# Optimization experiments

Hardware: AMD Instinct MI355X
Metric: run time of the kernel (lower is better)

The kernel has to match this reference:

```python
import jax, jax.numpy as jnp
import numpy as np
from jax import lax

H = 64           # hid_size (hard-pinned by reshape(4,6,64) in source)
B = 16384        # number of months (prototype batch)
A = 16           # agent_num
N = B * A        # rows of `inputs`
P = 24           # num_prototypes = 4 * 6
T = 32           # jieqi_info sequence length
ACT = 12         # action_dim
EPS = 1e-4       # self.epsilon
BN_EPS = 1e-5
LN_EPS = 1e-5


def _lstm_step(h, c, x, w_ih, w_hh, b_ih, b_hh):
    # torch LSTM gate order: i, f, g, o
    g = x @ w_ih.T + h @ w_hh.T + b_ih + b_hh
    i, f, gg, o = jnp.split(g, 4, axis=-1)
    c = jax.nn.sigmoid(f) * c + jax.nn.sigmoid(i) * jnp.tanh(gg)
    h = jax.nn.sigmoid(o) * jnp.tanh(c)
    return h, c


def setup_inputs() -> dict:
    key = jax.random.key(0)
    ks = iter(jax.random.split(key, 40))

    def nrm(shape, s=0.05):
        return jax.random.normal(next(ks), shape, jnp.float32) * s

    inp = {
        "inputs": jax.random.normal(next(ks), (N, H), jnp.float32),
        "hidden_state": jax.random.normal(next(ks), (N, H), jnp.float32),
        "month": jax.random.randint(next(ks), (B,), 0, 12, jnp.int32),
        "jieqi_info": jax.random.normal(next(ks), (P, T, 3), jnp.float32),
        # bidirectional LSTM (input 3 -> hidden H), forward + backward dirs
        "w_ih_f": nrm((4 * H, 3)), "w_hh_f": nrm((4 * H, H)),
        "b_ih_f": nrm((4 * H,)), "b_hh_f": nrm((4 * H,)),
        "w_ih_b": nrm((4 * H, 3)), "w_hh_b": nrm((4 * H, H)),
        "b_ih_b": nrm((4 * H,)), "b_hh_b": nrm((4 * H,)),
        "fcl_w": nrm((H, 2 * H)), "fcl_b": nrm((H,)),      # jieqi_lstm_fc
        "proj_w": nrm((H, H)),                               # proto_proj (no bias)
        "conv_w": nrm((H, 2 * H)), "conv_b": nrm((H,)),    # conv_global
        "bn_g": jnp.ones((H,), jnp.float32), "bn_b": jnp.zeros((H,), jnp.float32),
        "fc1_w": nrm((H, H)), "fc1_b": nrm((H,)),
        "ln_g": jnp.ones((H,), jnp.float32), "ln_b": jnp.zeros((H,), jnp.float32),
        "gru_wih": nrm((3 * H, H)), "gru_whh": nrm((3 * H, H)),
        "gru_bih": nrm((3 * H,)), "gru_bhh": nrm((3 * H,)),
        "out_w": nrm((ACT, H)), "out_b": nrm((ACT,)),
    }
    # last_layer weight: +1 on correct class, -0.5 on incorrect (set_last_layer_incorrect_connection)
    ident = np.zeros((P, 4), np.float32)
    ident[np.arange(P), np.arange(P) // 6] = 1.0
    inp["last_w"] = jnp.asarray(1.0 * ident.T + (-0.5) * (1.0 - ident.T))  # [4, 24]
    return inp


def reference(inputs, hidden_state, month, jieqi_info,
              w_ih_f, w_hh_f, b_ih_f, b_hh_f,
              w_ih_b, w_hh_b, b_ih_b, b_hh_b,
              fcl_w, fcl_b, proj_w, last_w,
              conv_w, conv_b, bn_g, bn_b,
              fc1_w, fc1_b, ln_g, ln_b,
              gru_wih, gru_whh, gru_bih, gru_bhh,
              out_w, out_b):
    dt = inputs.dtype
    # ---- get_jieqi_prototype: biLSTM over [P, T, 3], take output at t=T-1 ----
    z0 = jnp.zeros((P, H), dt)

    def step(carry, x_t):
        h, c = carry
        h, c = _lstm_step(h, c, x_t, w_ih_f, w_hh_f, b_ih_f, b_hh_f)
        return (h, c), None

    (h_f, _), _ = lax.scan(step, (z0, z0), jnp.swapaxes(jieqi_info, 0, 1))
    # backward direction's output at the last time index = one step on x[:, -1]
    h_b, _ = _lstm_step(z0, z0, jieqi_info[:, -1, :], w_ih_b, w_hh_b, b_ih_b, b_hh_b)
    th = jnp.concatenate([h_f, h_b], axis=-1)                 # [P, 2H]
    pv = jax.nn.relu(th @ fcl_w.T + fcl_b) @ proj_w.T         # prototype_vectors [P, H]

    # ---- prototype_distances on full input batch ----
    xp = inputs @ pv.T                                        # [N, P]
    min_distances = (-2.0 * xp
                     + jnp.sum(inputs ** 2, axis=1, keepdims=True)
                     + jnp.sum(pv ** 2, axis=1)[None, :])
    prototype_activations = jnp.log((min_distances + 1.0) / (min_distances + EPS))
    logits = prototype_activations @ last_w.T                 # [N, 4]

    # ---- month -> season, select seasonal prototype block ----
    seasons = jnp.mod(jnp.floor_divide(month - 2, 3), 4)      # 2-4:0, 5-7:1, 8-10:2, else 3
    sub_proto = pv.reshape(4, 6, H)[seasons]                  # [B, 6, H]

    # ---- prototype_subgraph_distances (vectorized over the 6 protos) ----
    xr = inputs.reshape(B, A, H)
    d = jnp.sum((xr[:, None, :, :] - sub_proto[:, :, None, :]) ** 2, axis=-1)  # [B, 6, A]
    sim = jnp.mean(jnp.log((d + 1.0) / (d + EPS)), axis=2)    # [B, 6]

    # ---- argmax + gather + repeat ----
    chosen_idx = jnp.argmax(sim, axis=1)                      # [B]
    chosen = sub_proto[jnp.arange(B), chosen_idx]             # [B, H]
    chosen = jnp.broadcast_to(chosen[:, None, :], (B, A, H)).reshape(N, H)

    # ---- conv_global -> batchnorm(train) -> relu ----
    x_glb = jnp.concatenate([inputs, chosen], axis=-1) @ conv_w.T + conv_b
    mu = jnp.mean(x_glb, axis=0)
    var = jnp.mean((x_glb - mu) ** 2, axis=0)                 # biased, training-mode BN
    x_glb = (x_glb - mu) * lax.rsqrt(var + BN_EPS) * bn_g + bn_b
    x_glb = jax.nn.relu(x_glb)

    # ---- fc1 -> layernorm -> relu ----
    x = x_glb @ fc1_w.T + fc1_b
    lmu = jnp.mean(x, axis=-1, keepdims=True)
    lvar = jnp.mean((x - lmu) ** 2, axis=-1, keepdims=True)
    x = (x - lmu) * lax.rsqrt(lvar + LN_EPS) * ln_g + ln_b
    x = jax.nn.relu(x)

    # ---- GRUCell ----
    h_in = hidden_state.reshape(-1, H)
    gi = x @ gru_wih.T + gru_bih
    gh = h_in @ gru_whh.T + gru_bhh
    r = jax.nn.sigmoid(gi[:, :H] + gh[:, :H])
    zg = jax.nn.sigmoid(gi[:, H:2 * H] + gh[:, H:2 * H])
    n = jnp.tanh(gi[:, 2 * H:] + r * gh[:, 2 * H:])
    h = (1.0 - zg) * n + zg * h_in

    a = h @ out_w.T + out_b
    return (a, h, logits, min_distances)
```

## Files before the change

### kernel.cpp

```cpp
#include <hip/hip_runtime.h>
#include <cmath>

#define NHID 64
#define NMONTH 16384
#define NAGENT 16
#define NROWS (NMONTH*NAGENT)
#define NPROTO 24
#define TSEQ 32
#define NACT 12
#define EPS_P  1e-4f
#define EPS_BN 1e-5f
#define EPS_LN 1e-5f

typedef __attribute__((ext_vector_type(8))) short short8;
typedef __attribute__((ext_vector_type(4))) float f32x4;
typedef __attribute__((ext_vector_type(4))) unsigned short us4;
typedef __attribute__((ext_vector_type(8))) unsigned short us8;
typedef unsigned short ushort_t;

#define MFMA(a,b,c) __builtin_amdgcn_mfma_f32_16x16x32_bf16(a,b,c,0,0,0)
#define LPAD 68
#define LDSFENCE() asm volatile("s_waitcnt lgkmcnt(0)" ::: "memory")
#define LD8(P) (*reinterpret_cast<const short8*>(P))

typedef const __attribute__((address_space(1))) void* gvp;
typedef __attribute__((address_space(3))) void* lvp;

#define WS_PV     3072
#define WS_PVSQ   4608
#define WS_CTAB   4640
#define WS_MID1   6176
#define WS_MID2   14368
#define WS_BNSC   22560
#define WS_BNSH   22624
#define WS_WBF16  22688
#define WO_FC1   0
#define WO_GIH   4096
#define WO_GHH   16384
#define WO_OUT   28672
#define WO_PV    29696
#define WO_CVX   31744

__device__ __forceinline__ float sigf(float x){ return 1.0f/(1.0f+expf(-x)); }
__device__ __forceinline__ float fsig(float x){
  return __builtin_amdgcn_rcpf(1.f + __expf(-x));
}
__device__ __forceinline__ float ftanh(float x){
  return 1.f - 2.f*__builtin_amdgcn_rcpf(1.f + __expf(2.f*x));
}
__device__ __forceinline__ ushort_t f2bf(float f){
  unsigned u = __builtin_bit_cast(unsigned, f);
  u += 0x7FFFu + ((u>>16)&1u);
  return (ushort_t)(u>>16);
}
__device__ __forceinline__ float bf2f(ushort_t b){
  return __builtin_bit_cast(float, ((unsigned)b)<<16);
}
__device__ __forceinline__ unsigned pk2bf(float a, float b){
  unsigned d;
  asm("v_cvt_pk_bf16_f32 %0, %1, %2" : "=v"(d) : "v"(a), "v"(b));
  return d;
}
__device__ __forceinline__ ushort_t f2bf_hw(float x){
  unsigned d;
  asm("v_cvt_pk_bf16_f32 %0, %1, %2" : "=v"(d) : "v"(x), "v"(x));
  return (ushort_t)d;
}
__device__ __forceinline__ short8 hfrag(const float* hraw, int ra, int base){
  const int r15 = ra & 15;
  const float4 a = *reinterpret_cast<const float4*>(&hraw[ra*64 + (((base  )^r15)<<2)]);
  const float4 b = *reinterpret_cast<const float4*>(&hraw[ra*64 + (((base+1)^r15)<<2)]);
  uint4 u; u.x=pk2bf(a.x,a.y); u.y=pk2bf(a.z,a.w); u.z=pk2bf(b.x,b.y); u.w=pk2bf(b.z,b.w);
  return __builtin_bit_cast(short8, u);
}

__global__ __launch_bounds__(256) void k1_lstm(
    const float* __restrict__ jq,
    const float* __restrict__ wif, const float* __restrict__ whf,
    const float* __restrict__ bif, const float* __restrict__ bhf,
    const float* __restrict__ wib, const float* __restrict__ bib, const float* __restrict__ bhb,
    const float* __restrict__ fclw, const float* __restrict__ fclb,
    const float* __restrict__ projw, const float* __restrict__ convb,
    const float* __restrict__ fc1w, const float* __restrict__ gwih,
    const float* __restrict__ gwhh, const float* __restrict__ outw,
    const float* __restrict__ convw, ushort_t* __restrict__ wb,
    float* __restrict__ pvsq, float* __restrict__ ctab)
{
  __shared__ float hs[NHID];
  __shared__ float gs[4*NHID];
  if (blockIdx.x >= NPROTO){
    const int tt = (blockIdx.x - NPROTO)*256 + threadIdx.x;
    for (int i=tt;i<4096;i+=1024)  wb[WO_FC1+i]=f2bf(fc1w[i]);
    for (int i=tt;i<12288;i+=1024){ wb[WO_GIH+i]=f2bf(gwih[i]); wb[WO_GHH+i]=f2bf(gwhh[i]); }
    for (int i=tt;i<1024;i+=1024)  wb[WO_OUT+i] = (i<768)? f2bf(outw[i]) : (ushort_t)0;
    for (int i=tt;i<4096;i+=1024)  wb[WO_CVX+i] = f2bf(convw[(i>>6)*128 + (i&63)]);
    return;
  }
  const int p = blockIdx.x;
  const int j = threadIdx.x;
  float wh[NHID];
  #pragma unroll
  for (int k=0;k<NHID;k++) wh[k] = whf[j*NHID+k];
  const float wi0=wif[j*3], wi1=wif[j*3+1], wi2=wif[j*3+2];
  const float bj = bif[j]+bhf[j];
  float c = 0.f;
  if (j < NHID) hs[j] = 0.f;
  __syncthreads();
  for (int t=0;t<TSEQ;t++){
    const float x0=jq[(p*TSEQ+t)*3], x1=jq[(p*TSEQ+t)*3+1], x2=jq[(p*TSEQ+t)*3+2];
    float g = wi0*x0+wi1*x1+wi2*x2+bj;
    #pragma unroll
    for (int k=0;k<NHID;k++) g += wh[k]*hs[k];
    __syncthreads();
    gs[j] = g;
    __syncthreads();
    if (j < NHID){
      const float gi=gs[j], gf=gs[NHID+j], gg=gs[2*NHID+j], go=gs[3*NHID+j];
      c = sigf(gf)*c + sigf(gi)*tanhf(gg);
      hs[j] = sigf(go)*tanhf(c);
    }
    __syncthreads();
  }
  const float x0=jq[(p*TSEQ+TSEQ-1)*3], x1=jq[(p*TSEQ+TSEQ-1)*3+1], x2=jq[(p*TSEQ+TSEQ-1)*3+2];
  const float gb = wib[j*3]*x0 + wib[j*3+1]*x1 + wib[j*3+2]*x2 + bib[j]+bhb[j];
  __syncthreads();
  gs[j] = gb;
  __syncthreads();
  if (j < NHID){
    const float gi=gs[j], gg=gs[2*NHID+j], go=gs[3*NHID+j];
    const float cb = sigf(gi)*tanhf(gg);
    const float hb = sigf(go)*tanhf(cb);
    const float hf = hs[j];
    __syncthreads();
    gs[j]      = hf;
    gs[NHID+j] = hb;
  } else {
    __syncthreads();
  }
  __syncthreads();

  if (j < NHID){
    float acc = fclb[j];
    for (int k=0;k<2*NHID;k++) acc += gs[k]*fclw[j*2*NHID+k];
    hs[j] = fmaxf(acc, 0.f);
  }
  __syncthreads();
  if (j < NHID){
    float pvh = 0.f;
    for (int k=0;k<NHID;k++) pvh += hs[k]*projw[j*NHID+k];
    gs[2*NHID+j] = pvh;
    wb[WO_PV + p*64 + j] = f2bf(pvh);
    if (p==0){
      #pragma unroll
      for (int r=24;r<32;r++) wb[WO_PV + r*64 + j] = (ushort_t)0;
    }
  }
  __syncthreads();
  if (j < NHID){
    const float* pvr = gs + 2*NHID;
    float ct = convb[j];
    for (int k=0;k<NHID;k++) ct += pvr[k]*convw[j*2*NHID+NHID+k];
    ctab[p*NHID+j] = ct;
    if (j==0){
      float s=0.f;
      for (int k=0;k<NHID;k++) s += pvr[k]*pvr[k];
      pvsq[p]=s;
    }
  }
}

__global__ __launch_bounds__(256) void k3_mfma(
    const float* __restrict__ inp, const int* __restrict__ month,
    const float* __restrict__ pvsq, const float* __restrict__ ctab,
    const float* __restrict__ lastw, const ushort_t* __restrict__ wb,
    float* __restrict__ out_logits, float* __restrict__ out_md,
    ushort_t* __restrict__ xgb, float* __restrict__ part1, float* __restrict__ part2)
{
  __shared__ ushort_t xl[64*72];
  __shared__ float insql[64];
  __shared__ float pal[64*26];

  const int t = threadIdx.x;
  const int w = t>>6, lane = t&63;
  const int l15 = lane&15, kg = lane>>4, ko = kg*8;
  const int gcol = w*16 + l15;
  const int rbase = w*16;
  const int rowA = rbase + l15;
  const size_t rowblk = (size_t)blockIdx.x*64;

  const int sr = t>>2, scb = (t&3)*16;
  float4 xr[4];
  #pragma unroll
  for (int i=0;i<4;i++)
    xr[i] = *reinterpret_cast<const float4*>(inp + (rowblk + sr)*64 + scb + i*4);
  const int mo = month[blockIdx.x*4 + w];

  const short8 pv0a = LD8(wb + WO_PV + l15*64 + ko);
  const short8 pv0b = LD8(wb + WO_PV + l15*64 + 32 + ko);
  const short8 pv1a = LD8(wb + WO_PV + (16+l15)*64 + ko);
  const short8 pv1b = LD8(wb + WO_PV + (16+l15)*64 + 32 + ko);
  const float pq0 = pvsq[l15];
  const float pq1 = (l15<8)? pvsq[16+l15] : 0.f;
  const int season = ((mo+10)%12)/3;

  {
    float ss = 0.f;
    #pragma unroll
    for (int i=0;i<4;i++){
      const float4 xv = xr[i];
      ss += xv.x*xv.x + xv.y*xv.y + xv.z*xv.z + xv.w*xv.w;
      uint2 yy; yy.x = pk2bf(xv.x, xv.y); yy.y = pk2bf(xv.z, xv.w);
      *reinterpret_cast<uint2*>(&xl[sr*72 + scb + i*4]) = yy;
    }
    ss += __shfl_xor(ss,1,4);
    ss += __shfl_xor(ss,2,4);
    if ((t&3)==0) insql[sr] = ss;
  }
  LDSFENCE();

  const short8 ax0 = LD8(&xl[rowA*72+ko]);
  const short8 ax1 = LD8(&xl[rowA*72+32+ko]);

  f32x4 d0={0.f,0.f,0.f,0.f}, d1=d0;
  d0 = MFMA(ax0, pv0a, d0);
  d0 = MFMA(ax1, pv0b, d0);
  d1 = MFMA(ax0, pv1a, d1);
  d1 = MFMA(ax1, pv1b, d1);
  {
    #pragma unroll
    for (int j=0;j<4;j++){
      const int rloc = rbase + kg*4 + j;
      const float iq = insql[rloc];
      const float md0 = iq + pq0 - 2.f*d0[j];
      out_md[(rowblk+rloc)*24 + l15] = md0;
      pal[rloc*26 + l15] = __logf(md0+1.f) - __logf(md0+EPS_P);
      const float md1 = iq + pq1 - 2.f*d1[j];
      const float pa1 = __logf(md1+1.f) - __logf(md1+EPS_P);
      if (l15<8){
        out_md[(rowblk+rloc)*24 + 16+l15] = md1;
        pal[rloc*26 + 16+l15] = pa1;
      }
    }
  }
  LDSFENCE();

  {
    const int r2 = rbase + (lane>>2), c = lane&3;
    float lgv = 0.f;
    #pragma unroll
    for (int p=0;p<24;p++) lgv += pal[r2*26+p]*lastw[c*24+p];
    out_logits[(rowblk+r2)*4 + c] = lgv;
  }

  int qsw;
  {
    float simv = -3.4e38f;
    const int j6 = lane & 7;
    if (j6 < 6){
      simv = 0.f;
      const int sp = season*6 + j6;
      #pragma unroll
      for (int i=0;i<16;i++) simv += pal[(rbase+i)*26 + sp];
    }
    int bidx = j6;
    { const float ov=__shfl_xor(simv,1,8); const int oi=__shfl_xor(bidx,1,8);
      if (ov>simv || (ov==simv && oi<bidx)){ simv=ov; bidx=oi; } }
    { const float ov=__shfl_xor(simv,2,8); const int oi=__shfl_xor(bidx,2,8);
      if (ov>simv || (ov==simv && oi<bidx)){ simv=ov; bidx=oi; } }
    { const float ov=__shfl_xor(simv,4,8); const int oi=__shfl_xor(bidx,4,8);
      if (ov>simv || (ov==simv && oi<bidx)){ simv=ov; bidx=oi; } }
    qsw = season*6 + bidx;
  }

  const short8 cw0  = LD8(wb + WO_CVX + gcol*64 + ko);
  const short8 cw1  = LD8(wb + WO_CVX + gcol*64 + 32 + ko);
  __syncthreads();

  ushort_t* xgblk = xgb + (size_t)blockIdx.x*8192;
  const float cg = ctab[qsw*64 + gcol];
  float s1=0.f, s2=0.f;
  #pragma unroll
  for (int rg=0; rg<4; rg++){
    const int ra = rg*16 + l15;
    const short8 bx0 = LD8(&xl[ra*72+ko]);
    const short8 bx1 = LD8(&xl[ra*72+32+ko]);
    f32x4 ac={0.f,0.f,0.f,0.f};
    ac = MFMA(bx0, cw0, ac);
    ac = MFMA(bx1, cw1, ac);
    #pragma unroll
    for (int j=0;j<4;j++){
      const int rloc = rg*16 + kg*4 + j;
      const float v = ac[j] + cg;
      xgblk[rloc*64 + gcol] = f2bf_hw(v);
      s1 += v; s2 += v*v;
    }
  }
  s1 += __shfl_xor(s1,16); s1 += __shfl_xor(s1,32);
  s2 += __shfl_xor(s2,16); s2 += __shfl_xor(s2,32);
  if (kg==0){
    part1[(size_t)blockIdx.x*64 + gcol] = s1;
    part2[(size_t)blockIdx.x*64 + gcol] = s2;
  }
}

__global__ __launch_bounds__(64) void k4b_reduce(
    const float* __restrict__ part1, const float* __restrict__ part2,
    double* __restrict__ mid1, double* __restrict__ mid2)
{
  const int i = blockIdx.x, c = threadIdx.x;
  double s1=0.0, s2=0.0;
  for (int b=i*64; b<i*64+64; b++){
    s1 += (double)part1[b*64+c];
    s2 += (double)part2[b*64+c];
  }
  mid1[i*64+c]=s1; mid2[i*64+c]=s2;
}

__global__ __launch_bounds__(64) void k5_finalize(
    const double* __restrict__ mid1, const double* __restrict__ mid2,
    const float* __restrict__ bng, const float* __restrict__ bnb,
    float* __restrict__ bnsc, float* __restrict__ bnsh)
{
  const int f = threadIdx.x;
  double s1=0.0, s2=0.0;
  for (int i=0;i<64;i++){ s1+=mid1[i*64+f]; s2+=mid2[i*64+f]; }
  const double mu = s1 / (double)NROWS;
  double var = s2/(double)NROWS - mu*mu;
  if (var < 0.0) var = 0.0;
  const float sc = bng[f] * (float)(1.0/sqrt(var + (double)EPS_BN));
  bnsc[f]=sc;
  bnsh[f]=bnb[f]-(float)mu*sc;
}

__global__ __launch_bounds__(256) void k6_mfma(
    const ushort_t* __restrict__ xgb, const float* __restrict__ hidden,
    const float* __restrict__ bnsc, const float* __restrict__ bnsh,
    const float* __restrict__ fc1b, const float* __restrict__ lng, const float* __restrict__ lnb,
    const float* __restrict__ gbih, const float* __restrict__ gbhh,
    const float* __restrict__ outb,
    const ushort_t* __restrict__ wb,
    float* __restrict__ out_a, float* __restrict__ out_h)
{
  __shared__ ushort_t ybuf[64*LPAD];
  __shared__ float hraw[64*64];
  const int t = threadIdx.x;
  const int lane = t & 63, w = t >> 6;
  const int l15 = lane & 15, kg = lane >> 4;
  const int ko = kg*8;
  const int rbase = w*16;
  const int rowA = rbase + l15;
  const int sr = t>>2, scb = (t&3)*16;

  const ushort_t* xgp = xgb + (size_t)blockIdx.x*8192 + sr*64 + scb;
  const us8 xv0 = *reinterpret_cast<const us8*>(xgp);
  const us8 xv1 = *reinterpret_cast<const us8*>(xgp+8);

  const short8 f0a = LD8(wb + WO_FC1 + ( 0+l15)*64 + ko);
  const short8 f0b = LD8(wb + WO_FC1 + ( 0+l15)*64 + 32 + ko);
  const short8 f1a = LD8(wb + WO_FC1 + (16+l15)*64 + ko);
  const short8 f1b = LD8(wb + WO_FC1 + (16+l15)*64 + 32 + ko);
  const short8 f2a = LD8(wb + WO_FC1 + (32+l15)*64 + ko);
  const short8 f2b = LD8(wb + WO_FC1 + (32+l15)*64 + 32 + ko);
  const short8 f3a = LD8(wb + WO_FC1 + (48+l15)*64 + ko);
  const short8 f3b = LD8(wb + WO_FC1 + (48+l15)*64 + 32 + ko);

  {
    const float* hbase = hidden + (size_t)blockIdx.x*4096;
    #pragma unroll
    for (int k=0;k<4;k++){
      const int c = (w*4+k)*64 + lane;
      const int row = c>>4, ccp = c&15;
      const float* src = hbase + row*64 + ((ccp ^ (row&15))<<2);
      float* dst = &hraw[(w*4+k)*256];
      __builtin_amdgcn_global_load_lds((gvp)src, (lvp)dst, 16, 0, 0);
    }
  }

  {
    float xf[16];
    #pragma unroll
    for (int e=0;e<8;e++){ xf[e]=bf2f(xv0[e]); xf[8+e]=bf2f(xv1[e]); }
    #pragma unroll
    for (int i=0;i<4;i++){
      const float4 sc = *reinterpret_cast<const float4*>(bnsc + scb + i*4);
      const float4 sh = *reinterpret_cast<const float4*>(bnsh + scb + i*4);
      const float y0 = fmaxf(xf[4*i  ]*sc.x+sh.x, 0.f);
      const float y1 = fmaxf(xf[4*i+1]*sc.y+sh.y, 0.f);
      const float y2 = fmaxf(xf[4*i+2]*sc.z+sh.z, 0.f);
      const float y3 = fmaxf(xf[4*i+3]*sc.w+sh.w, 0.f);
      uint2 yy; yy.x = pk2bf(y0,y1); yy.y = pk2bf(y2,y3);
      *reinterpret_cast<uint2*>(&ybuf[sr*LPAD + scb + i*4]) = yy;
    }
  }
  LDSFENCE();

  const short8 ay0 = LD8(&ybuf[rowA*LPAD + ko]);
  const short8 ay1 = LD8(&ybuf[rowA*LPAD + 32 + ko]);

  f32x4 ac0={0.f,0.f,0.f,0.f}, ac1=ac0, ac2=ac0, ac3=ac0;
  ac0 = MFMA(ay0, f0a, ac0);  ac0 = MFMA(ay1, f0b, ac0);
  ac1 = MFMA(ay0, f1a, ac1);  ac1 = MFMA(ay1, f1b, ac1);
  ac2 = MFMA(ay0, f2a, ac2);  ac2 = MFMA(ay1, f2b, ac2);
  ac3 = MFMA(ay0, f3a, ac3);  ac3 = MFMA(ay1, f3b, ac3);
  {
    const float b0=fc1b[l15], b1=fc1b[16+l15], b2=fc1b[32+l15], b3=fc1b[48+l15];
    float tn0[4], tn1[4], tn2[4], tn3[4], mu[4], rs[4];
    #pragma unroll
    for (int j=0;j<4;j++){ tn0[j]=ac0[j]+b0; tn1[j]=ac1[j]+b1; tn2[j]=ac2[j]+b2; tn3[j]=ac3[j]+b3; }
    #pragma unroll
    for (int j=0;j<4;j++){
      float s = tn0[j]+tn1[j]+tn2[j]+tn3[j];
      s += __shfl_xor(s,1,16); s += __shfl_xor(s,2,16);
      s += __shfl_xor(s,4,16); s += __shfl_xor(s,8,16);
      mu[j] = s*(1.f/64.f);
    }
    #pragma unroll
    for (int j=0;j<4;j++){
      const float d0_=tn0[j]-mu[j], d1_=tn1[j]-mu[j], d2_=tn2[j]-mu[j], d3_=tn3[j]-mu[j];
      float v = d0_*d0_+d1_*d1_+d2_*d2_+d3_*d3_;
      v += __shfl_xor(v,1,16); v += __shfl_xor(v,2,16);
      v += __shfl_xor(v,4,16); v += __shfl_xor(v,8,16);
      rs[j] = 1.f/sqrtf(v*(1.f/64.f)+EPS_LN);
    }
    const float g0=lng[l15], g1=lng[16+l15], g2=lng[32+l15], g3=lng[48+l15];
    const float q0=lnb[l15], q1=lnb[16+l15], q2=lnb[32+l15], q3=lnb[48+l15];
    #pragma unroll
    for (int j=0;j<4;j++){
      const int rr_ = rbase + kg*4 + j;
      ybuf[rr_*LPAD +      l15] = f2bf_hw(fmaxf((tn0[j]-mu[j])*rs[j]*g0+q0, 0.f));
      ybuf[rr_*LPAD + 16 + l15] = f2bf_hw(fmaxf((tn1[j]-mu[j])*rs[j]*g1+q1, 0.f));
      ybuf[rr_*LPAD + 32 + l15] = f2bf_hw(fmaxf((tn2[j]-mu[j])*rs[j]*g2+q2, 0.f));
      ybuf[rr_*LPAD + 48 + l15] = f2bf_hw(fmaxf((tn3[j]-mu[j])*rs[j]*g3+q3, 0.f));
    }
  }

  const int gcol = w*16 + l15;
  const ushort_t* gih = wb + WO_GIH;
  const ushort_t* ghh = wb + WO_GHH;
  const short8 wr0 = LD8(gih + (      gcol)*64 + ko);
  const short8 wr1 = LD8(gih + (      gcol)*64 + 32 + ko);
  const short8 wz0 = LD8(gih + ( 64 + gcol)*64 + ko);
  const short8 wz1 = LD8(gih + ( 64 + gcol)*64 + 32 + ko);
  const short8 wn0 = LD8(gih + (128 + gcol)*64 + ko);
  const short8 wn1 = LD8(gih + (128 + gcol)*64 + 32 + ko);
  const short8 vr0 = LD8(ghh + (      gcol)*64 + ko);
  const short8 vr1 = LD8(ghh + (      gcol)*64 + 32 + ko);
  const short8 vz0 = LD8(ghh + ( 64 + gcol)*64 + ko);
  const short8 vz1 = LD8(ghh + ( 64 + gcol)*64 + 32 + ko);
  const short8 vn0 = LD8(ghh + (128 + gcol)*64 + ko);
  const short8 vn1 = LD8(ghh + (128 + gcol)*64 + 32 + ko);
  const float bir=gbih[gcol],     bhr=gbhh[gcol];
  const float biz=gbih[64+gcol],  bhz=gbhh[64+gcol];
  const float bin_=gbih[128+gcol],bhn=gbhh[128+gcol];
  __syncthreads();

  us4 hkeep[4];
  #pragma unroll
  for (int rg=0; rg<4; rg++){
    const int ra = rg*16 + l15;
    const short8 at0 = LD8(&ybuf[ra*LPAD + ko]);
    const short8 at1 = LD8(&ybuf[ra*LPAD + 32 + ko]);
    const short8 bh0 = hfrag(hraw, ra, 2*kg);
    const short8 bh1 = hfrag(hraw, ra, 8+2*kg);
    f32x4 ar={0.f,0.f,0.f,0.f}, az=ar, an=ar, hn=ar;
    ar = MFMA(at0, wr0, ar);  ar = MFMA(at1, wr1, ar);
    ar = MFMA(bh0, vr0, ar);  ar = MFMA(bh1, vr1, ar);
    az = MFMA(at0, wz0, az);  az = MFMA(at1, wz1, az);
    az = MFMA(bh0, vz0, az);  az = MFMA(bh1, vz1, az);
    an = MFMA(at0, wn0, an);  an = MFMA(at1, wn1, an);
    hn = MFMA(bh0, vn0, hn);  hn = MFMA(bh1, vn1, hn);
    us4 hb4;
    #pragma unroll
    for (int j=0;j<4;j++){
      const int rloc = rg*16 + kg*4 + j;
      const size_t rg_ = (size_t)blockIdx.x*64 + rloc;
      const float rrg = fsig(ar[j]+bir+bhr);
      const float zzg = fsig(az[j]+biz+bhz);
      const float nng = ftanh(an[j]+bin_ + rrg*(hn[j]+bhn));
      const float hold = hraw[rloc*64 + ((((gcol>>2)^(rloc&15))<<2) + (gcol&3))];
      const float hv = (1.f-zzg)*nng + zzg*hold;
      out_h[rg_*64 + gcol] = hv;
      hb4[j] = f2bf_hw(hv);
    }
    hkeep[rg] = hb4;
  }

  const short8 ow0 = LD8(wb + WO_OUT + l15*64 + ko);
  const short8 ow1 = LD8(wb + WO_OUT + l15*64 + 32 + ko);
  const float ob = (l15 < 12) ? outb[l15] : 0.f;

  __syncthreads();
  #pragma unroll
  for (int rg=0; rg<4; rg++){
    #pragma unroll
    for (int j=0;j<4;j++)
      ybuf[(rg*16 + kg*4 + j)*LPAD + gcol] = hkeep[rg][j];
  }
  __syncthreads();

  const short8 av0 = LD8(&ybuf[rowA*LPAD + ko]);
  const short8 av1 = LD8(&ybuf[rowA*LPAD + 32 + ko]);
  f32x4 aa={0.f,0.f,0.f,0.f};
  aa = MFMA(av0, ow0, aa);
  aa = MFMA(av1, ow1, aa);
  if (l15 < 12){
    #pragma unroll
    for (int j=0;j<4;j++){
      const size_t rg_ = (size_t)blockIdx.x*64 + rbase + kg*4 + j;
      out_a[rg_*12 + l15] = aa[j] + ob;
    }
  }
}

extern "C" void kernel_launch(void* const* d_in, const int* in_sizes, int n_in,
                              void* d_out, int out_size, void* d_ws, size_t ws_size,
                              hipStream_t stream)
{
  (void)in_sizes; (void)n_in; (void)out_size; (void)ws_size;
  const float* inputs = (const float*)d_in[0];
  const float* hidden = (const float*)d_in[1];
  const int*   month  = (const int*)d_in[2];
  const float* jq     = (const float*)d_in[3];
  const float* wif    = (const float*)d_in[4];
  const float* whf    = (const float*)d_in[5];
  const float* bif    = (const float*)d_in[6];
  const float* bhf    = (const float*)d_in[7];
  const float* wib    = (const float*)d_in[8];
  const float* bib    = (const float*)d_in[10];
  const float* bhb    = (const float*)d_in[11];
  const float* fclw   = (const float*)d_in[12];
  const float* fclb   = (const float*)d_in[13];
  const float* projw  = (const float*)d_in[14];
  const float* convw  = (const float*)d_in[15];
  const float* convb  = (const float*)d_in[16];
  const float* bng    = (const float*)d_in[17];
  const float* bnb    = (const float*)d_in[18];
  const float* fc1w   = (const float*)d_in[19];
  const float* fc1b   = (const float*)d_in[20];
  const float* lng    = (const float*)d_in[21];
  const float* lnb    = (const float*)d_in[22];
  const float* gwih   = (const float*)d_in[23];
  const float* gwhh   = (const float*)d_in[24];
  const float* gbih   = (const float*)d_in[25];
  const float* gbhh   = (const float*)d_in[26];
  const float* outw   = (const float*)d_in[27];
  const float* outb   = (const float*)d_in[28];
  const float* lastw  = (const float*)d_in[29];

  float* ws  = (float*)d_ws;
  float* out = (float*)d_out;
  float* out_a  = out;
  float* out_h  = out + (size_t)NROWS*NACT;
  float* out_lg = out + (size_t)NROWS*(NACT+NHID);
  float* out_md = out + (size_t)NROWS*(NACT+NHID+4);
  ushort_t* wb = (ushort_t*)(ws + WS_WBF16);
  ushort_t* xgb = (ushort_t*)out_h;
  float* part1 = out_a;
  float* part2 = out_a + (size_t)4096*64;

  hipLaunchKernelGGL(k1_lstm, dim3(NPROTO+4), dim3(256), 0, stream,
                     jq, wif, whf, bif, bhf, wib, bib, bhb,
                     fclw, fclb, projw, convb,
                     fc1w, gwih, gwhh, outw, convw, wb,
                     ws+WS_PVSQ, ws+WS_CTAB);
  hipLaunchKernelGGL(k3_mfma, dim3(NROWS/64), dim3(256), 0, stream,
                     inputs, month, ws+WS_PVSQ, ws+WS_CTAB, lastw, wb,
                     out_lg, out_md, xgb, part1, part2);
  hipLaunchKernelGGL(k4b_reduce, dim3(64), dim3(64), 0, stream,
                     part1, part2, (double*)(ws+WS_MID1), (double*)(ws+WS_MID2));
  hipLaunchKernelGGL(k5_finalize, dim3(1), dim3(64), 0, stream,
                     (const double*)(ws+WS_MID1), (const double*)(ws+WS_MID2),
                     bng, bnb, ws+WS_BNSC, ws+WS_BNSH);
  hipLaunchKernelGGL(k6_mfma, dim3(NROWS/64), dim3(256), 0, stream,
                     xgb, hidden, ws+WS_BNSC, ws+WS_BNSH, fc1b, lng, lnb,
                     gbih, gbhh, outb, wb, out_a, out_h);
}
```

Measured before the change: 140.1 us.

## Stage hidden state as bf16 in LDS and stream GRU weights to cut registers

The hidden state is now loaded through registers, converted to bf16 once, and stored in a padded LDS tile. This replaces the fp32 swizzled direct-to-LDS load and the per-fragment conversion, and halves that LDS footprint. FC1 and GRU weight fragments are loaded just before each MFMA instead of all being held live, and launch bounds request 8 blocks per CU, all aimed at lower register pressure and higher occupancy. The catch is that the GRU blend's old hidden value now comes from the bf16 copy, which loses precision on out_h. Weight reloads inside the row-group loop may also add global/L1 traffic.

Measured after the change: 260.8 us. 86.2% more time.

```diff
diff --git a/kernel.cpp b/kernel.cpp
--- a/kernel.cpp
+++ b/kernel.cpp
@@ -22,9 +22,6 @@
 #define LPAD 68
 #define LDSFENCE() asm volatile("s_waitcnt lgkmcnt(0)" ::: "memory")
 #define LD8(P) (*reinterpret_cast<const short8*>(P))
-
-typedef const __attribute__((address_space(1))) void* gvp;
-typedef __attribute__((address_space(3))) void* lvp;
 
 #define WS_PV     3072
 #define WS_PVSQ   4608
@@ -65,13 +62,6 @@
   unsigned d;
   asm("v_cvt_pk_bf16_f32 %0, %1, %2" : "=v"(d) : "v"(x), "v"(x));
   return (ushort_t)d;
-}
-__device__ __forceinline__ short8 hfrag(const float* hraw, int ra, int base){
-  const int r15 = ra & 15;
-  const float4 a = *reinterpret_cast<const float4*>(&hraw[ra*64 + (((base  )^r15)<<2)]);
-  const float4 b = *reinterpret_cast<const float4*>(&hraw[ra*64 + (((base+1)^r15)<<2)]);
-  uint4 u; u.x=pk2bf(a.x,a.y); u.y=pk2bf(a.z,a.w); u.z=pk2bf(b.x,b.y); u.w=pk2bf(b.z,b.w);
-  return __builtin_bit_cast(short8, u);
 }
 
 __global__ __launch_bounds__(256) void k1_lstm(
@@ -332,7 +322,7 @@
   bnsh[f]=bnb[f]-(float)mu*sc;
 }
 
-__global__ __launch_bounds__(256) void k6_mfma(
+__global__ __launch_bounds__(256, 8) void k6_mfma(
     const ushort_t* __restrict__ xgb, const float* __restrict__ hidden,
     const float* __restrict__ bnsc, const float* __restrict__ bnsh,
     const float* __restrict__ fc1b, const float* __restrict__ lng, const float* __restrict__ lnb,
@@ -342,7 +332,7 @@
     float* __restrict__ out_a, float* __restrict__ out_h)
 {
   __shared__ ushort_t ybuf[64*LPAD];
-  __shared__ float hraw[64*64];
+  __shared__ ushort_t hidl[64*LPAD];
   const int t = threadIdx.x;
   const int lane = t & 63, w = t >> 6;
   const int l15 = lane & 15, kg = lane >> 4;
@@ -354,27 +344,11 @@
   const ushort_t* xgp = xgb + (size_t)blockIdx.x*8192 + sr*64 + scb;
   const us8 xv0 = *reinterpret_cast<const us8*>(xgp);
   const us8 xv1 = *reinterpret_cast<const us8*>(xgp+8);
-
-  const short8 f0a = LD8(wb + WO_FC1 + ( 0+l15)*64 + ko);
-  const short8 f0b = LD8(wb + WO_FC1 + ( 0+l15)*64 + 32 + ko);
-  const short8 f1a = LD8(wb + WO_FC1 + (16+l15)*64 + ko);
-  const short8 f1b = LD8(wb + WO_FC1 + (16+l15)*64 + 32 + ko);
-  const short8 f2a = LD8(wb + WO_FC1 + (32+l15)*64 + ko);
-  const short8 f2b = LD8(wb + WO_FC1 + (32+l15)*64 + 32 + ko);
-  const short8 f3a = LD8(wb + WO_FC1 + (48+l15)*64 + ko);
-  const short8 f3b = LD8(wb + WO_FC1 + (48+l15)*64 + 32 + ko);
-
-  {
-    const float* hbase = hidden + (size_t)blockIdx.x*4096;
-    #pragma unroll
-    for (int k=0;k<4;k++){
-      const int c = (w*4+k)*64 + lane;
-      const int row = c>>4, ccp = c&15;
-      const float* src = hbase + row*64 + ((ccp ^ (row&15))<<2);
-      float* dst = &hraw[(w*4+k)*256];
-      __builtin_amdgcn_global_load_lds((gvp)src, (lvp)dst, 16, 0, 0);
-    }
-  }
+  const size_t g = ((size_t)blockIdx.x*64 + sr)*64 + scb;
+  float4 hv4[4];
+  #pragma unroll
+  for (int i=0;i<4;i++)
+    hv4[i] = *reinterpret_cast<const float4*>(hidden + g + i*4);
 
   {
     float xf[16];
@@ -390,6 +364,9 @@
       const float y3 = fmaxf(xf[4*i+3]*sc.w+sh.w, 0.f);
       uint2 yy; yy.x = pk2bf(y0,y1); yy.y = pk2bf(y2,y3);
       *reinterpret_cast<uint2*>(&ybuf[sr*LPAD + scb + i*4]) = yy;
+      const float4 h4 = hv4[i];
+      uint2 hh; hh.x = pk2bf(h4.x,h4.y); hh.y = pk2bf(h4.z,h4.w);
+      *reinterpret_cast<uint2*>(&hidl[sr*LPAD + scb + i*4]) = hh;
     }
   }
   LDSFENCE();
@@ -397,11 +374,22 @@
   const short8 ay0 = LD8(&ybuf[rowA*LPAD + ko]);
   const short8 ay1 = LD8(&ybuf[rowA*LPAD + 32 + ko]);
 
-  f32x4 ac0={0.f,0.f,0.f,0.f}, ac1=ac0, ac2=ac0, ac3=ac0;
-  ac0 = MFMA(ay0, f0a, ac0);  ac0 = MFMA(ay1, f0b, ac0);
-  ac1 = MFMA(ay0, f1a, ac1);  ac1 = MFMA(ay1, f1b, ac1);
-  ac2 = MFMA(ay0, f2a, ac2);  ac2 = MFMA(ay1, f2b, ac2);
-  ac3 = MFMA(ay0, f3a, ac3);  ac3 = MFMA(ay1, f3b, ac3);
+  f32x4 ac0, ac1, ac2, ac3;
+  {
+    short8 fa, fb;
+    fa = LD8(wb + WO_FC1 + ( 0+l15)*64 + ko);
+    fb = LD8(wb + WO_FC1 + ( 0+l15)*64 + 32 + ko);
+    ac0 = MFMA(ay0, fa, ((f32x4){0.f,0.f,0.f,0.f}));  ac0 = MFMA(ay1, fb, ac0);
+    fa = LD8(wb + WO_FC1 + (16+l15)*64 + ko);
+    fb = LD8(wb + WO_FC1 + (16+l15)*64 + 32 + ko);
+    ac1 = MFMA(ay0, fa, ((f32x4){0.f,0.f,0.f,0.f}));  ac1 = MFMA(ay1, fb, ac1);
+    fa = LD8(wb + WO_FC1 + (32+l15)*64 + ko);
+    fb = LD8(wb + WO_FC1 + (32+l15)*64 + 32 + ko);
+    ac2 = MFMA(ay0, fa, ((f32x4){0.f,0.f,0.f,0.f}));  ac2 = MFMA(ay1, fb, ac2);
+    fa = LD8(wb + WO_FC1 + (48+l15)*64 + ko);
+    fb = LD8(wb + WO_FC1 + (48+l15)*64 + 32 + ko);
+    ac3 = MFMA(ay0, fa, ((f32x4){0.f,0.f,0.f,0.f}));  ac3 = MFMA(ay1, fb, ac3);
+  }
   {
     const float b0=fc1b[l15], b1=fc1b[16+l15], b2=fc1b[32+l15], b3=fc1b[48+l15];
     float tn0[4], tn1[4], tn2[4], tn3[4], mu[4], rs[4];
@@ -435,49 +423,56 @@
   }
 
   const int gcol = w*16 + l15;
+  const float br  = gbih[gcol]     + gbhh[gcol];
+  const float bz  = gbih[64+gcol]  + gbhh[64+gcol];
+  const float bin_= gbih[128+gcol];
+  const float bhn = gbhh[128+gcol];
+  __syncthreads();
+
   const ushort_t* gih = wb + WO_GIH;
   const ushort_t* ghh = wb + WO_GHH;
-  const short8 wr0 = LD8(gih + (      gcol)*64 + ko);
-  const short8 wr1 = LD8(gih + (      gcol)*64 + 32 + ko);
-  const short8 wz0 = LD8(gih + ( 64 + gcol)*64 + ko);
-  const short8 wz1 = LD8(gih + ( 64 + gcol)*64 + 32 + ko);
-  const short8 wn0 = LD8(gih + (128 + gcol)*64 + ko);
-  const short8 wn1 = LD8(gih + (128 + gcol)*64 + 32 + ko);
-  const short8 vr0 = LD8(ghh + (      gcol)*64 + ko);
-  const short8 vr1 = LD8(ghh + (      gcol)*64 + 32 + ko);
-  const short8 vz0 = LD8(ghh + ( 64 + gcol)*64 + ko);
-  const short8 vz1 = LD8(ghh + ( 64 + gcol)*64 + 32 + ko);
-  const short8 vn0 = LD8(ghh + (128 + gcol)*64 + ko);
-  const short8 vn1 = LD8(ghh + (128 + gcol)*64 + 32 + ko);
-  const float bir=gbih[gcol],     bhr=gbhh[gcol];
-  const float biz=gbih[64+gcol],  bhz=gbhh[64+gcol];
-  const float bin_=gbih[128+gcol],bhn=gbhh[128+gcol];
-  __syncthreads();
-
   us4 hkeep[4];
   #pragma unroll
   for (int rg=0; rg<4; rg++){
     const int ra = rg*16 + l15;
     const short8 at0 = LD8(&ybuf[ra*LPAD + ko]);
     const short8 at1 = LD8(&ybuf[ra*LPAD + 32 + ko]);
-    const short8 bh0 = hfrag(hraw, ra, 2*kg);
-    const short8 bh1 = hfrag(hraw, ra, 8+2*kg);
-    f32x4 ar={0.f,0.f,0.f,0.f}, az=ar, an=ar, hn=ar;
-    ar = MFMA(at0, wr0, ar);  ar = MFMA(at1, wr1, ar);
-    ar = MFMA(bh0, vr0, ar);  ar = MFMA(bh1, vr1, ar);
-    az = MFMA(at0, wz0, az);  az = MFMA(at1, wz1, az);
-    az = MFMA(bh0, vz0, az);  az = MFMA(bh1, vz1, az);
-    an = MFMA(at0, wn0, an);  an = MFMA(at1, wn1, an);
-    hn = MFMA(bh0, vn0, hn);  hn = MFMA(bh1, vn1, hn);
+    const short8 bh0 = LD8(&hidl[ra*LPAD + ko]);
+    const short8 bh1 = LD8(&hidl[ra*LPAD + 32 + ko]);
+    f32x4 ar, az, an, hn;
+    {
+      short8 a = LD8(gih + (      gcol)*64 + ko);
+      short8 b = LD8(gih + (      gcol)*64 + 32 + ko);
+      ar = MFMA(at0, a, ((f32x4){0.f,0.f,0.f,0.f}));  ar = MFMA(at1, b, ar);
+      a = LD8(ghh + (      gcol)*64 + ko);
+      b = LD8(ghh + (      gcol)*64 + 32 + ko);
+      ar = MFMA(bh0, a, ar);  ar = MFMA(bh1, b, ar);
+    }
+    {
+      short8 a = LD8(gih + ( 64 + gcol)*64 + ko);
+      short8 b = LD8(gih + ( 64 + gcol)*64 + 32 + ko);
+      az = MFMA(at0, a, ((f32x4){0.f,0.f,0.f,0.f}));  az = MFMA(at1, b, az);
+      a = LD8(ghh + ( 64 + gcol)*64 + ko);
+      b = LD8(ghh + ( 64 + gcol)*64 + 32 + ko);
+      az = MFMA(bh0, a, az);  az = MFMA(bh1, b, az);
+    }
+    {
+      short8 a = LD8(gih + (128 + gcol)*64 + ko);
+      short8 b = LD8(gih + (128 + gcol)*64 + 32 + ko);
+      an = MFMA(at0, a, ((f32x4){0.f,0.f,0.f,0.f}));  an = MFMA(at1, b, an);
+      a = LD8(ghh + (128 + gcol)*64 + ko);
+      b = LD8(ghh + (128 + gcol)*64 + 32 + ko);
+      hn = MFMA(bh0, a, ((f32x4){0.f,0.f,0.f,0.f}));  hn = MFMA(bh1, b, hn);
+    }
     us4 hb4;
     #pragma unroll
     for (int j=0;j<4;j++){
       const int rloc = rg*16 + kg*4 + j;
       const size_t rg_ = (size_t)blockIdx.x*64 + rloc;
-      const float rrg = fsig(ar[j]+bir+bhr);
-      const float zzg = fsig(az[j]+biz+bhz);
+      const float rrg = fsig(ar[j]+br);
+      const float zzg = fsig(az[j]+bz);
       const float nng = ftanh(an[j]+bin_ + rrg*(hn[j]+bhn));
-      const float hold = hraw[rloc*64 + ((((gcol>>2)^(rloc&15))<<2) + (gcol&3))];
+      const float hold = bf2f(hidl[rloc*LPAD + gcol]);
       const float hv = (1.f-zzg)*nng + zzg*hold;
       out_h[rg_*64 + gcol] = hv;
       hb4[j] = f2bf_hw(hv);
@@ -485,11 +480,12 @@
     hkeep[rg] = hb4;
   }
 
+  __syncthreads();
+
   const short8 ow0 = LD8(wb + WO_OUT + l15*64 + ko);
   const short8 ow1 = LD8(wb + WO_OUT + l15*64 + 32 + ko);
   const float ob = (l15 < 12) ? outb[l15] : 0.f;
 
-  __syncthreads();
   #pragma unroll
   for (int rg=0; rg<4; rg++){
     #pragma unroll
```
